# Kernel optimization log

Measured on AMD Instinct MI355X. Metric: run time of the kernel, lower is better.

The kernel has to match this reference:

```python
import jax, jax.numpy as jnp
import numpy as np

N = 50000      # nodes
E = 1600000    # edges
F_IN = 128     # input_dim
H = 160        # hidden_dim
G = 512        # graphs in batch
C = 2          # num_classes
EPS = 1e-5     # BatchNorm eps


def setup_inputs() -> dict:
    key = jax.random.key(0)
    ks = jax.random.split(key, 12)
    x = jax.random.normal(ks[0], (N, F_IN), jnp.float32)
    edge_index = jax.random.randint(ks[1], (2, E), 0, N, dtype=jnp.int32)
    batch = jnp.sort(jax.random.randint(ks[2], (N,), 0, G, dtype=jnp.int32))

    def lin(k, fi, fo):
        s = 1.0 / np.sqrt(fi)
        kw, kb = jax.random.split(k)
        W = jax.random.uniform(kw, (fi, fo), jnp.float32, -s, s)
        b = jax.random.uniform(kb, (fo,), jnp.float32, -s, s)
        return W, b

    W1, b1 = lin(ks[3], F_IN, H)
    W2, b2 = lin(ks[4], H, H)
    W3, b3 = lin(ks[5], H, H)
    Wc1, bc1 = lin(ks[6], H, H // 2)
    Wc2, bc2 = lin(ks[7], H // 2, C)

    def bn(k):
        k1, k2, k3, k4 = jax.random.split(k, 4)
        gamma = jax.random.uniform(k1, (H,), jnp.float32, 0.5, 1.5)
        beta = jax.random.normal(k2, (H,), jnp.float32) * 0.1
        mean = jax.random.normal(k3, (H,), jnp.float32) * 0.1
        var = jax.random.uniform(k4, (H,), jnp.float32, 0.5, 1.5)
        return gamma, beta, mean, var

    g1, be1, m1, v1 = bn(ks[8])
    g2, be2, m2, v2 = bn(ks[9])
    g3, be3, m3, v3 = bn(ks[10])

    return dict(x=x, edge_index=edge_index, batch=batch,
                W1=W1, b1=b1, W2=W2, b2=b2, W3=W3, b3=b3,
                g1=g1, be1=be1, m1=m1, v1=v1,
                g2=g2, be2=be2, m2=m2, v2=v2,
                g3=g3, be3=be3, m3=m3, v3=v3,
                Wc1=Wc1, bc1=bc1, Wc2=Wc2, bc2=bc2)


def gcn_conv(x, W, b, src, dst):
    """PyG GCNConv: symmetric deg normalization with self-loops; lin -> aggregate -> +bias."""
    n = x.shape[0]
    h = x @ W                                   # [N, H]
    loop = jnp.arange(n, dtype=src.dtype)
    s = jnp.concatenate([src, loop])            # self-loops appended
    d = jnp.concatenate([dst, loop])
    deg = jax.ops.segment_sum(jnp.ones_like(d, jnp.float32), d, num_segments=n)
    inv = jnp.where(deg > 0, jax.lax.rsqrt(deg), 0.0)
    msg = h[s] * (inv[s] * inv[d])[:, None]     # [E+N, H] gather + norm
    return jax.ops.segment_sum(msg, d, num_segments=n) + b


def bn_eval(x, gamma, beta, mean, var):
    return (x - mean) * jax.lax.rsqrt(var + EPS) * gamma + beta


def reference(x, edge_index, batch, W1, b1, W2, b2, W3, b3,
              g1, be1, m1, v1, g2, be2, m2, v2, g3, be3, m3, v3,
              Wc1, bc1, Wc2, bc2):
    src, dst = edge_index[0], edge_index[1]
    # eval mode: dropout is identity, BN uses running stats
    h = jax.nn.relu(bn_eval(gcn_conv(x, W1, b1, src, dst), g1, be1, m1, v1))
    h = jax.nn.relu(bn_eval(gcn_conv(h, W2, b2, src, dst), g2, be2, m2, v2))
    h = jax.nn.relu(bn_eval(gcn_conv(h, W3, b3, src, dst), g3, be3, m3, v3))
    # global mean pool over graph ids
    sums = jax.ops.segment_sum(h, batch, num_segments=G)
    cnt = jax.ops.segment_sum(jnp.ones((h.shape[0],), jnp.float32), batch, num_segments=G)
    pooled = sums / jnp.clip(cnt, 1.0)[:, None]
    # MLP head
    z = jax.nn.relu(pooled @ Wc1 + bc1)
    return z @ Wc2 + bc2
```

## Files before the change

kernel.cpp:

```cpp
#include <hip/hip_runtime.h>

#define N_NODES   50000
#define N_EDGES   1600000
#define FDIM_IN   128
#define HDIM      160
#define N_GRAPHS  512
#define BN_EPS    1e-5f
#define NBKT_MAX  128
#define HIST_BLOCKS 256

typedef short  frag8 __attribute__((ext_vector_type(8)));
typedef float  facc4 __attribute__((ext_vector_type(4)));


__device__ __forceinline__ unsigned short f2bf(float f) {
    unsigned int u = __float_as_uint(f);
    return (unsigned short)((u + 0x7FFFu + ((u >> 16) & 1u)) >> 16);
}

__device__ __forceinline__ unsigned int pack2(float lo, float hi) {
    return (unsigned int)f2bf(lo) | ((unsigned int)f2bf(hi) << 16);
}

__device__ __forceinline__ void addpk(float* acc, uint4 r) {
    acc[0] += __uint_as_float(r.x << 16);
    acc[1] += __uint_as_float(r.x & 0xFFFF0000u);
    acc[2] += __uint_as_float(r.y << 16);
    acc[3] += __uint_as_float(r.y & 0xFFFF0000u);
    acc[4] += __uint_as_float(r.z << 16);
    acc[5] += __uint_as_float(r.z & 0xFFFF0000u);
    acc[6] += __uint_as_float(r.w << 16);
    acc[7] += __uint_as_float(r.w & 0xFFFF0000u);
}


__global__ __launch_bounds__(256) void coarse_hist_kernel(const int* __restrict__ dst,
                                                          int* __restrict__ cg, int E) {
    __shared__ int h[NBKT_MAX];
    int tid = threadIdx.x;
    if (tid < NBKT_MAX) h[tid] = 0;
    __syncthreads();
    for (int e = blockIdx.x * 256 + tid; e < E; e += gridDim.x * 256)
        atomicAdd(&h[dst[e] >> 9], 1);
    __syncthreads();
    if (tid < NBKT_MAX) cg[blockIdx.x * NBKT_MAX + tid] = h[tid];
}


struct PrepArgs {
    const float *b, *g, *be, *m, *v;
    float *sc, *sh;
};

__global__ __launch_bounds__(256) void setup_kernel(const int* __restrict__ cg,
                                                    int* __restrict__ bucket_base,
                                                    int* __restrict__ bucket_cursor,
                                                    PrepArgs a0, PrepArgs a1, PrepArgs a2,
                                                    const float* __restrict__ W1,
                                                    const float* __restrict__ W2,
                                                    const float* __restrict__ W3,
                                                    unsigned short* __restrict__ o1,
                                                    unsigned short* __restrict__ o2,
                                                    unsigned short* __restrict__ o3) {
    int bid = blockIdx.x;
    int t = threadIdx.x;
    if (bid == 0) {
        __shared__ int h[NBKT_MAX];
        __shared__ int total;
        if (t < NBKT_MAX) {
            int s = 0;
            for (int b = 0; b < HIST_BLOCKS; ++b) s += cg[b * NBKT_MAX + t];
            h[t] = s;
        }
        __syncthreads();
        if (t == 0) {
            int run = 0;
            for (int i = 0; i < NBKT_MAX; ++i) { int c = h[i]; h[i] = run; run += c; }
            total = run;
        }
        __syncthreads();
        if (t < NBKT_MAX) {
            bucket_base[t] = h[t];
            bucket_cursor[t] = h[t];
        }
        if (t == 0) bucket_base[NBKT_MAX] = total;
    } else if (bid <= 3) {
        PrepArgs a = (bid == 1) ? a0 : (bid == 2) ? a1 : a2;
        if (t < HDIM) {
            float s = a.g[t] * rsqrtf(a.v[t] + BN_EPS);
            a.sc[t] = s;
            a.sh[t] = (a.b[t] - a.m[t]) * s + a.be[t];
        }
    } else {
        int i = (bid - 4) * 256 + t;
        const float* W;
        unsigned short* o;
        if (i < 128 * 160)                 { W = W1; o = o1; }
        else if (i < 128 * 160 + 160 * 160) { W = W2; o = o2; i -= 128 * 160; }
        else if (i < 128 * 160 + 2 * 160 * 160) { W = W3; o = o3; i -= 128 * 160 + 160 * 160; }
        else return;
        int j = i & 7;
        int l = (i >> 3) & 63;
        int u = (i >> 9) % 10;
        int tt = i / 5120;
        int k = tt * 32 + (l >> 4) * 8 + j;
        int nn = u * 16 + (l & 15);
        o[i] = f2bf(W[k * 160 + nn]);
    }
}

__global__ __launch_bounds__(256) void part_kernel(const int* __restrict__ src,
                                                   const int* __restrict__ dst,
                                                   int* __restrict__ bucket_cursor,
                                                   unsigned int* __restrict__ pairs, int E) {
    __shared__ int bcnt[NBKT_MAX], bbase[NBKT_MAX], lc[NBKT_MAX];
    int tid = threadIdx.x;
    int per = (E + gridDim.x - 1) / gridDim.x;
    int beg = blockIdx.x * per;
    int end = min(beg + per, E);
    if (tid < NBKT_MAX) { bcnt[tid] = 0; lc[tid] = 0; }
    __syncthreads();
    for (int e = beg + tid; e < end; e += 256)
        atomicAdd(&bcnt[dst[e] >> 9], 1);
    __syncthreads();
    if (tid < NBKT_MAX)
        bbase[tid] = bcnt[tid] ? atomicAdd(&bucket_cursor[tid], bcnt[tid]) : 0;
    __syncthreads();
    for (int e = beg + tid; e < end; e += 256) {
        int d = dst[e];
        int b = d >> 9;
        int pos = bbase[b] + atomicAdd(&lc[b], 1);
        pairs[pos] = ((unsigned int)src[e] << 9) | (unsigned int)(d & 511);
    }
}

__global__ __launch_bounds__(1024) void bucket_csr_kernel(const unsigned int* __restrict__ pairs,
                                                          const int* __restrict__ bucket_base,
                                                          int* __restrict__ row_off,
                                                          float* __restrict__ inv,
                                                          int* __restrict__ ssrc,
                                                          const float* __restrict__ x,
                                                          unsigned short* __restrict__ xs,
                                                          int n) {
    __shared__ int h[512];
    __shared__ int ws[8];
    __shared__ float sinv[512];
    int tid = threadIdx.x;
    int b = blockIdx.x;
    int node0 = b << 9;
    int beg = bucket_base[b], end = bucket_base[b + 1];
    if (tid < 512) h[tid] = 0;
    __syncthreads();
    for (int j = beg + tid; j < end; j += 1024)
        atomicAdd(&h[pairs[j] & 511], 1);
    __syncthreads();
    int cntv = (tid < 512) ? h[tid] : 0;
    __syncthreads();
    int lane = tid & 63, wid = tid >> 6;
    int incl = cntv;
    #pragma unroll
    for (int off = 1; off < 64; off <<= 1) {
        int u = __shfl_up(incl, off);
        if (lane >= off) incl += u;
    }
    if (tid < 512 && lane == 63) ws[wid] = incl;
    __syncthreads();
    if (tid == 0) {
        int r = 0;
        #pragma unroll
        for (int i = 0; i < 8; ++i) { int t = ws[i]; ws[i] = r; r += t; }
    }
    __syncthreads();
    int excl = (tid < 512) ? (ws[wid] + incl - cntv) : 0;
    if (tid < 512) {
        float iv = rsqrtf((float)(cntv + 1));
        int node = node0 + tid;
        if (node < n) {
            row_off[node] = beg + excl;
            inv[node] = iv;
        }
        sinv[tid] = iv;
        h[tid] = excl;
    }
    if (tid == 0 && (node0 + 512) >= n) row_off[n] = end;
    __syncthreads();
    for (int j = beg + tid; j < end; j += 1024) {
        unsigned int p = pairs[j];
        int pos = beg + atomicAdd(&h[p & 511], 1);
        ssrc[pos] = (int)(p >> 9);
    }
    for (int idx = tid; idx < 512 * 32; idx += 1024) {
        int nd = node0 + (idx >> 5);
        if (nd < n) {
            float w = sinv[idx >> 5];
            float4 v = ((const float4*)x)[(size_t)nd * 32 + (idx & 31)];
            ushort4 o;
            o.x = f2bf(v.x * w); o.y = f2bf(v.y * w);
            o.z = f2bf(v.z * w); o.w = f2bf(v.w * w);
            ((ushort4*)xs)[(size_t)nd * 32 + (idx & 31)] = o;
        }
    }
}


template <int C>
__global__ __launch_bounds__(256) void agg_grp_kernel(const unsigned short* __restrict__ in_s,
                                                      const float* __restrict__ inv,
                                                      const int* __restrict__ row_off,
                                                      const int* __restrict__ ssrc,
                                                      unsigned short* __restrict__ out, int n) {
    constexpr int LPR = C / 8;
    constexpr int G   = 64 / LPR;
    constexpr int RB  = C * 2;
    int wave = threadIdx.x >> 6;
    int lane = threadIdx.x & 63;
    int node = blockIdx.x * 4 + wave;
    if (node >= n) return;
    int g  = lane / LPR;
    int cl = lane - g * LPR;
    bool act = g < G;
    int beg = row_off[node], end = row_off[node + 1];
    const char* base = (const char*)in_s;
    int lb = cl * 16;

    float acc[8];
    #pragma unroll
    for (int i = 0; i < 8; ++i) acc[i] = 0.f;

    if (g == 0) {
        uint4 r = *(const uint4*)(base + (size_t)node * RB + lb);
        addpk(acc, r);
    }

    int e = act ? beg + g : end;
    for (; e + G < end; e += 2 * G) {
        int s0 = ssrc[e], s1 = ssrc[e + G];
        uint4 r0 = *(const uint4*)(base + (size_t)s0 * RB + lb);
        uint4 r1 = *(const uint4*)(base + (size_t)s1 * RB + lb);
        addpk(acc, r0);
        addpk(acc, r1);
    }
    if (e < end) {
        uint4 r = *(const uint4*)(base + (size_t)ssrc[e] * RB + lb);
        addpk(acc, r);
    }

    if (G == 4) {
        #pragma unroll
        for (int i = 0; i < 8; ++i) acc[i] += __shfl(acc[i], lane + 32);
        #pragma unroll
        for (int i = 0; i < 8; ++i) acc[i] += __shfl(acc[i], lane + 16);
    } else {
        #pragma unroll
        for (int i = 0; i < 8; ++i) {
            float a = __shfl(acc[i], lane + 20);
            float b = __shfl(acc[i], lane + 40);
            acc[i] += a + b;
        }
    }

    if (lane < LPR) {
        float wi = inv[node];
        uint4 o;
        o.x = pack2(acc[0] * wi, acc[1] * wi);
        o.y = pack2(acc[2] * wi, acc[3] * wi);
        o.z = pack2(acc[4] * wi, acc[5] * wi);
        o.w = pack2(acc[6] * wi, acc[7] * wi);
        *(uint4*)((char*)out + (size_t)node * RB + lb) = o;
    }
}


template <int K, int OUTMODE>
__global__ __launch_bounds__(256) void mfma_gemm_kernel(const unsigned short* __restrict__ A,
                                                        const unsigned short* __restrict__ Bp,
                                                        const float* __restrict__ sc,
                                                        const float* __restrict__ sh,
                                                        const float* __restrict__ inv,
                                                        float* __restrict__ CoutF,
                                                        unsigned short* __restrict__ CoutB,
                                                        int n) {
    constexpr int KT = K / 32;
    int tid = threadIdx.x;
    int wave = tid >> 6, lane = tid & 63;
    int row0 = blockIdx.x * 64 + wave * 16;
    int m = lane & 15, q = lane >> 4;

    int arow = row0 + m;
    int arowc = (arow < n) ? arow : (n - 1);
    const frag8* Abase = (const frag8*)(A + (size_t)arowc * K);
    const frag8* Bbase = (const frag8*)Bp;

    facc4 acc[10];
    #pragma unroll
    for (int u = 0; u < 10; ++u) acc[u] = (facc4){0.f, 0.f, 0.f, 0.f};

    #pragma unroll
    for (int t = 0; t < KT; ++t) {
        frag8 af = Abase[t * 4 + q];
        #pragma unroll
        for (int u = 0; u < 10; ++u) {
            frag8 bf = Bbase[(t * 10 + u) * 64 + lane];
            acc[u] = __builtin_amdgcn_mfma_f32_16x16x32_bf16(af, bf, acc[u], 0, 0, 0);
        }
    }

    #pragma unroll
    for (int u = 0; u < 10; ++u) {
        int c = u * 16 + m;
        float scv = sc[c], shv = sh[c];
        #pragma unroll
        for (int r = 0; r < 4; ++r) {
            int rr = row0 + q * 4 + r;
            if (rr < n) {
                float v = fmaxf(acc[u][r] * scv + shv, 0.f);
                if (OUTMODE == 1) {
                    CoutB[(size_t)rr * 160 + c] = f2bf(v * inv[rr]);
                } else {
                    CoutF[(size_t)rr * 160 + c] = v;
                }
            }
        }
    }
}


__global__ __launch_bounds__(256) void pool_head_kernel(const float* __restrict__ h,
                                                        const int* __restrict__ batch,
                                                        const float* __restrict__ Wc1,
                                                        const float* __restrict__ bc1,
                                                        const float* __restrict__ Wc2,
                                                        const float* __restrict__ bc2,
                                                        float* __restrict__ out, int n) {
    __shared__ float pooled[160];
    __shared__ float z[80];
    __shared__ int range[2];
    int g = blockIdx.x;
    int t = threadIdx.x;
    if (t < 2) {
        int target = g + t;
        int lo = 0, hi = n;
        while (lo < hi) {
            int mid = (lo + hi) >> 1;
            if (batch[mid] < target) lo = mid + 1; else hi = mid;
        }
        range[t] = lo;
    }
    __syncthreads();
    int lo = range[0], hi = range[1];
    if (t < 160) {
        float s = 0.f;
        for (int r = lo; r < hi; ++r) s += h[(size_t)r * 160 + t];
        pooled[t] = s / fmaxf((float)(hi - lo), 1.f);
    }
    __syncthreads();
    if (t < 80) {
        float s = bc1[t];
        for (int k = 0; k < 160; ++k) s += pooled[k] * Wc1[k * 80 + t];
        z[t] = fmaxf(s, 0.f);
    }
    __syncthreads();
    if (t < 2) {
        float s = bc2[t];
        for (int k = 0; k < 80; ++k) s += z[k] * Wc2[k * 2 + t];
        out[g * 2 + t] = s;
    }
}


static inline size_t align256(size_t x) { return (x + 255) & ~(size_t)255; }

extern "C" void kernel_launch(void* const* d_in, const int* in_sizes, int n_in,
                              void* d_out, int out_size, void* d_ws, size_t ws_size,
                              hipStream_t stream) {
    const float* x   = (const float*)d_in[0];
    const int* ei    = (const int*)d_in[1];
    const int* batch = (const int*)d_in[2];
    const float* W1  = (const float*)d_in[3];
    const float* b1  = (const float*)d_in[4];
    const float* W2  = (const float*)d_in[5];
    const float* b2  = (const float*)d_in[6];
    const float* W3  = (const float*)d_in[7];
    const float* b3  = (const float*)d_in[8];
    const float* g1  = (const float*)d_in[9];
    const float* be1 = (const float*)d_in[10];
    const float* m1  = (const float*)d_in[11];
    const float* v1  = (const float*)d_in[12];
    const float* g2  = (const float*)d_in[13];
    const float* be2 = (const float*)d_in[14];
    const float* m2  = (const float*)d_in[15];
    const float* v2  = (const float*)d_in[16];
    const float* g3  = (const float*)d_in[17];
    const float* be3 = (const float*)d_in[18];
    const float* m3  = (const float*)d_in[19];
    const float* v3  = (const float*)d_in[20];
    const float* Wc1 = (const float*)d_in[21];
    const float* bc1 = (const float*)d_in[22];
    const float* Wc2 = (const float*)d_in[23];
    const float* bc2 = (const float*)d_in[24];
    float* out = (float*)d_out;

    const int N = in_sizes[2];
    const int E = in_sizes[1] / 2;
    const int* src = ei;
    const int* dst = ei + E;

    char* w = (char*)d_ws;
    int*   row_off = (int*)w;             w += align256((size_t)(N + 1) * 4);
    float* inv     = (float*)w;           w += align256((size_t)N * 4);
    int*   ssrc    = (int*)w;             w += align256((size_t)E * 4);
    unsigned int* pairs = (unsigned int*)w; w += align256((size_t)E * 4);
    int*   cg      = (int*)w;             w += align256((size_t)HIST_BLOCKS * NBKT_MAX * 4);
    int*   bucket_base   = (int*)w;       w += align256((size_t)(NBKT_MAX + 1) * 4);
    int*   bucket_cursor = (int*)w;       w += align256((size_t)NBKT_MAX * 4);
    float* scsh    = (float*)w;           w += align256((size_t)6 * HDIM * 4);
    unsigned short* W1p = (unsigned short*)w;  w += align256((size_t)FDIM_IN * HDIM * 2);
    unsigned short* W2p = (unsigned short*)w;  w += align256((size_t)HDIM * HDIM * 2);
    unsigned short* W3p = (unsigned short*)w;  w += align256((size_t)HDIM * HDIM * 2);
    unsigned short* bufA_bf = (unsigned short*)w;  w += align256((size_t)N * HDIM * 2);
    char* regionR = w;
    unsigned short* xs_bf = (unsigned short*)regionR;
    unsigned short* hs_bf = (unsigned short*)(regionR + align256((size_t)N * FDIM_IN * 2));
    float* bufB = (float*)regionR;
    float* sc1 = scsh, *sh1 = scsh + 160, *sc2 = scsh + 320, *sh2 = scsh + 480,
         * sc3 = scsh + 640, *sh3 = scsh + 800;

    coarse_hist_kernel<<<HIST_BLOCKS, 256, 0, stream>>>(dst, cg, E);

    PrepArgs pa0 = {b1, g1, be1, m1, v1, sc1, sh1};
    PrepArgs pa1 = {b2, g2, be2, m2, v2, sc2, sh2};
    PrepArgs pa2 = {b3, g3, be3, m3, v3, sc3, sh3};
    int packTotal = 128 * 160 + 2 * 160 * 160;
    int setupBlocks = 4 + (packTotal + 255) / 256;
    setup_kernel<<<setupBlocks, 256, 0, stream>>>(cg, bucket_base, bucket_cursor,
                                                  pa0, pa1, pa2, W1, W2, W3, W1p, W2p, W3p);

    part_kernel<<<256, 256, 0, stream>>>(src, dst, bucket_cursor, pairs, E);
    int nbkt = (N + 511) >> 9;
    bucket_csr_kernel<<<nbkt, 1024, 0, stream>>>(pairs, bucket_base, row_off, inv, ssrc, x, xs_bf, N);

    int gAgg = (N + 3) / 4;
    int gGemm = (N + 63) / 64;

    agg_grp_kernel<128><<<gAgg, 256, 0, stream>>>(xs_bf, inv, row_off, ssrc, bufA_bf, N);
    mfma_gemm_kernel<128, 1><<<gGemm, 256, 0, stream>>>(bufA_bf, W1p, sc1, sh1, inv, nullptr, hs_bf, N);
    agg_grp_kernel<160><<<gAgg, 256, 0, stream>>>(hs_bf, inv, row_off, ssrc, bufA_bf, N);
    mfma_gemm_kernel<160, 1><<<gGemm, 256, 0, stream>>>(bufA_bf, W2p, sc2, sh2, inv, nullptr, hs_bf, N);
    agg_grp_kernel<160><<<gAgg, 256, 0, stream>>>(hs_bf, inv, row_off, ssrc, bufA_bf, N);
    mfma_gemm_kernel<160, 0><<<gGemm, 256, 0, stream>>>(bufA_bf, W3p, sc3, sh3, inv, bufB, nullptr, N);

    pool_head_kernel<<<N_GRAPHS, 256, 0, stream>>>(bufB, batch, Wc1, bc1, Wc2, bc2, out, N);
}
```

Baseline: 466.4 us.

## Shrink CSR buckets, stage GEMM weights in LDS with two row tiles, parallelize pooling

Halves the bucket width to 256 nodes so twice as many blocks run the CSR build. The MFMA GEMM now copies the packed weight matrix into shared memory once per block and computes two 64-row tiles per block, reusing each B fragment across both tiles. The pooling kernel splits each graph's rows across 6 sub-groups with float4 loads before reducing, which adds parallelism in the per-graph sum. Risks are larger LDS use (up to about 51KB) and register pressure from doubled accumulators, both of which could lower occupancy.

```diff
diff --git a/kernel.cpp b/kernel.cpp
--- a/kernel.cpp
+++ b/kernel.cpp
@@ -6,8 +6,9 @@
 #define HDIM      160
 #define N_GRAPHS  512
 #define BN_EPS    1e-5f
-#define NBKT_MAX  128
-#define HIST_BLOCKS 256
+#define NBKT_MAX  256
+#define BKT_SH    8
+#define HIST_BLOCKS 128
 
 typedef short  frag8 __attribute__((ext_vector_type(8)));
 typedef float  facc4 __attribute__((ext_vector_type(4)));
@@ -41,7 +42,7 @@
     if (tid < NBKT_MAX) h[tid] = 0;
     __syncthreads();
     for (int e = blockIdx.x * 256 + tid; e < E; e += gridDim.x * 256)
-        atomicAdd(&h[dst[e] >> 9], 1);
+        atomicAdd(&h[dst[e] >> BKT_SH], 1);
     __syncthreads();
     if (tid < NBKT_MAX) cg[blockIdx.x * NBKT_MAX + tid] = h[tid];
 }
@@ -121,16 +122,16 @@
     if (tid < NBKT_MAX) { bcnt[tid] = 0; lc[tid] = 0; }
     __syncthreads();
     for (int e = beg + tid; e < end; e += 256)
-        atomicAdd(&bcnt[dst[e] >> 9], 1);
+        atomicAdd(&bcnt[dst[e] >> BKT_SH], 1);
     __syncthreads();
     if (tid < NBKT_MAX)
         bbase[tid] = bcnt[tid] ? atomicAdd(&bucket_cursor[tid], bcnt[tid]) : 0;
     __syncthreads();
     for (int e = beg + tid; e < end; e += 256) {
         int d = dst[e];
-        int b = d >> 9;
+        int b = d >> BKT_SH;
         int pos = bbase[b] + atomicAdd(&lc[b], 1);
-        pairs[pos] = ((unsigned int)src[e] << 9) | (unsigned int)(d & 511);
+        pairs[pos] = ((unsigned int)src[e] << BKT_SH) | (unsigned int)(d & (NBKT_MAX - 1));
     }
 }
 
@@ -142,19 +143,19 @@
                                                           const float* __restrict__ x,
                                                           unsigned short* __restrict__ xs,
                                                           int n) {
-    __shared__ int h[512];
-    __shared__ int ws[8];
-    __shared__ float sinv[512];
+    __shared__ int h[NBKT_MAX];
+    __shared__ int ws[4];
+    __shared__ float sinv[NBKT_MAX];
     int tid = threadIdx.x;
     int b = blockIdx.x;
-    int node0 = b << 9;
+    int node0 = b << BKT_SH;
     int beg = bucket_base[b], end = bucket_base[b + 1];
-    if (tid < 512) h[tid] = 0;
+    if (tid < NBKT_MAX) h[tid] = 0;
     __syncthreads();
     for (int j = beg + tid; j < end; j += 1024)
-        atomicAdd(&h[pairs[j] & 511], 1);
-    __syncthreads();
-    int cntv = (tid < 512) ? h[tid] : 0;
+        atomicAdd(&h[pairs[j] & (NBKT_MAX - 1)], 1);
+    __syncthreads();
+    int cntv = (tid < NBKT_MAX) ? h[tid] : 0;
     __syncthreads();
     int lane = tid & 63, wid = tid >> 6;
     int incl = cntv;
@@ -163,16 +164,16 @@
         int u = __shfl_up(incl, off);
         if (lane >= off) incl += u;
     }
-    if (tid < 512 && lane == 63) ws[wid] = incl;
+    if (tid < NBKT_MAX && lane == 63) ws[wid] = incl;
     __syncthreads();
     if (tid == 0) {
         int r = 0;
         #pragma unroll
-        for (int i = 0; i < 8; ++i) { int t = ws[i]; ws[i] = r; r += t; }
-    }
-    __syncthreads();
-    int excl = (tid < 512) ? (ws[wid] + incl - cntv) : 0;
-    if (tid < 512) {
+        for (int i = 0; i < 4; ++i) { int t = ws[i]; ws[i] = r; r += t; }
+    }
+    __syncthreads();
+    int excl = (tid < NBKT_MAX) ? (ws[wid] + incl - cntv) : 0;
+    if (tid < NBKT_MAX) {
         float iv = rsqrtf((float)(cntv + 1));
         int node = node0 + tid;
         if (node < n) {
@@ -182,14 +183,14 @@
         sinv[tid] = iv;
         h[tid] = excl;
     }
-    if (tid == 0 && (node0 + 512) >= n) row_off[n] = end;
+    if (tid == 0 && (node0 + NBKT_MAX) >= n) row_off[n] = end;
     __syncthreads();
     for (int j = beg + tid; j < end; j += 1024) {
         unsigned int p = pairs[j];
-        int pos = beg + atomicAdd(&h[p & 511], 1);
-        ssrc[pos] = (int)(p >> 9);
-    }
-    for (int idx = tid; idx < 512 * 32; idx += 1024) {
+        int pos = beg + atomicAdd(&h[p & (NBKT_MAX - 1)], 1);
+        ssrc[pos] = (int)(p >> BKT_SH);
+    }
+    for (int idx = tid; idx < NBKT_MAX * 32; idx += 1024) {
         int nd = node0 + (idx >> 5);
         if (nd < n) {
             float w = sinv[idx >> 5];
@@ -281,27 +282,40 @@
                                                         unsigned short* __restrict__ CoutB,
                                                         int n) {
     constexpr int KT = K / 32;
+    constexpr int BQ = K * 20;
+    __shared__ uint4 Bs[BQ];
     int tid = threadIdx.x;
+    for (int i = tid; i < BQ; i += 256) Bs[i] = ((const uint4*)Bp)[i];
+
     int wave = tid >> 6, lane = tid & 63;
-    int row0 = blockIdx.x * 64 + wave * 16;
     int m = lane & 15, q = lane >> 4;
-
-    int arow = row0 + m;
-    int arowc = (arow < n) ? arow : (n - 1);
-    const frag8* Abase = (const frag8*)(A + (size_t)arowc * K);
-    const frag8* Bbase = (const frag8*)Bp;
-
-    facc4 acc[10];
+    int row0 = blockIdx.x * 128 + wave * 16;
+    int row1 = row0 + 64;
+
+    int ar0 = row0 + m; ar0 = (ar0 < n) ? ar0 : (n - 1);
+    int ar1 = row1 + m; ar1 = (ar1 < n) ? ar1 : (n - 1);
+    const frag8* A0 = (const frag8*)(A + (size_t)ar0 * K);
+    const frag8* A1 = (const frag8*)(A + (size_t)ar1 * K);
+    const frag8* Bf = (const frag8*)Bs;
+
+    facc4 acc0[10], acc1[10];
     #pragma unroll
-    for (int u = 0; u < 10; ++u) acc[u] = (facc4){0.f, 0.f, 0.f, 0.f};
+    for (int u = 0; u < 10; ++u) {
+        acc0[u] = (facc4){0.f, 0.f, 0.f, 0.f};
+        acc1[u] = (facc4){0.f, 0.f, 0.f, 0.f};
+    }
+
+    __syncthreads();
 
     #pragma unroll
     for (int t = 0; t < KT; ++t) {
-        frag8 af = Abase[t * 4 + q];
+        frag8 af0 = A0[t * 4 + q];
+        frag8 af1 = A1[t * 4 + q];
         #pragma unroll
         for (int u = 0; u < 10; ++u) {
-            frag8 bf = Bbase[(t * 10 + u) * 64 + lane];
-            acc[u] = __builtin_amdgcn_mfma_f32_16x16x32_bf16(af, bf, acc[u], 0, 0, 0);
+            frag8 bf = Bf[(t * 10 + u) * 64 + lane];
+            acc0[u] = __builtin_amdgcn_mfma_f32_16x16x32_bf16(af0, bf, acc0[u], 0, 0, 0);
+            acc1[u] = __builtin_amdgcn_mfma_f32_16x16x32_bf16(af1, bf, acc1[u], 0, 0, 0);
         }
     }
 
@@ -313,12 +327,15 @@
         for (int r = 0; r < 4; ++r) {
             int rr = row0 + q * 4 + r;
             if (rr < n) {
-                float v = fmaxf(acc[u][r] * scv + shv, 0.f);
-                if (OUTMODE == 1) {
-                    CoutB[(size_t)rr * 160 + c] = f2bf(v * inv[rr]);
-                } else {
-                    CoutF[(size_t)rr * 160 + c] = v;
-                }
+                float v = fmaxf(acc0[u][r] * scv + shv, 0.f);
+                if (OUTMODE == 1) CoutB[(size_t)rr * 160 + c] = f2bf(v * inv[rr]);
+                else              CoutF[(size_t)rr * 160 + c] = v;
+            }
+            int rr1 = row1 + q * 4 + r;
+            if (rr1 < n) {
+                float v = fmaxf(acc1[u][r] * scv + shv, 0.f);
+                if (OUTMODE == 1) CoutB[(size_t)rr1 * 160 + c] = f2bf(v * inv[rr1]);
+                else              CoutF[(size_t)rr1 * 160 + c] = v;
             }
         }
     }
@@ -332,6 +349,7 @@
                                                         const float* __restrict__ Wc2,
                                                         const float* __restrict__ bc2,
                                                         float* __restrict__ out, int n) {
+    __shared__ float4 part[6][40];
     __shared__ float pooled[160];
     __shared__ float z[80];
     __shared__ int range[2];
@@ -348,10 +366,28 @@
     }
     __syncthreads();
     int lo = range[0], hi = range[1];
-    if (t < 160) {
-        float s = 0.f;
-        for (int r = lo; r < hi; ++r) s += h[(size_t)r * 160 + t];
-        pooled[t] = s / fmaxf((float)(hi - lo), 1.f);
+    int sub = t / 40, c4 = t - sub * 40;
+    if (sub < 6) {
+        float4 a = {0.f, 0.f, 0.f, 0.f};
+        for (int r = lo + sub; r < hi; r += 6) {
+            float4 v = ((const float4*)(h + (size_t)r * 160))[c4];
+            a.x += v.x; a.y += v.y; a.z += v.z; a.w += v.w;
+        }
+        part[sub][c4] = a;
+    }
+    __syncthreads();
+    if (t < 40) {
+        float4 s = {0.f, 0.f, 0.f, 0.f};
+        #pragma unroll
+        for (int i = 0; i < 6; ++i) {
+            float4 p = part[i][t];
+            s.x += p.x; s.y += p.y; s.z += p.z; s.w += p.w;
+        }
+        float ic = 1.f / fmaxf((float)(hi - lo), 1.f);
+        pooled[t * 4 + 0] = s.x * ic;
+        pooled[t * 4 + 1] = s.y * ic;
+        pooled[t * 4 + 2] = s.z * ic;
+        pooled[t * 4 + 3] = s.w * ic;
     }
     __syncthreads();
     if (t < 80) {
@@ -436,11 +472,11 @@
                                                   pa0, pa1, pa2, W1, W2, W3, W1p, W2p, W3p);
 
     part_kernel<<<256, 256, 0, stream>>>(src, dst, bucket_cursor, pairs, E);
-    int nbkt = (N + 511) >> 9;
+    int nbkt = (N + NBKT_MAX - 1) >> BKT_SH;
     bucket_csr_kernel<<<nbkt, 1024, 0, stream>>>(pairs, bucket_base, row_off, inv, ssrc, x, xs_bf, N);
 
     int gAgg = (N + 3) / 4;
-    int gGemm = (N + 63) / 64;
+    int gGemm = (N + 127) / 128;
 
     agg_grp_kernel<128><<<gAgg, 256, 0, stream>>>(xs_bf, inv, row_off, ssrc, bufA_bf, N);
     mfma_gemm_kernel<128, 1><<<gGemm, 256, 0, stream>>>(bufA_bf, W1p, sc1, sh1, inv, nullptr, hs_bf, N);
```

Measured after the change: 459.3 us. No clear change (-1.5%).
